# Kernel optimization log

Hardware: AMD Instinct MI355X
Metric: run time of the kernel (lower is better)

Reference implementation:

```python
import jax, jax.numpy as jnp
import numpy as np

N = 50000
E = 800000
D = 64


def sage_conv(x, src, dst, Wl, Wr, b, n_nodes):
    # message = x[src]; mean-aggregate by dst; then lin_l(mean) + lin_r(x) + b
    msg = x[src]                                             # [E, D] gather
    ssum = jax.ops.segment_sum(msg, dst, num_segments=n_nodes)  # [N, D]
    cnt = jax.ops.segment_sum(jnp.ones((msg.shape[0],), dtype=x.dtype), dst,
                              num_segments=n_nodes)          # [N]
    mean = ssum / jnp.maximum(cnt, 1.0)[:, None]             # scatter-mean (empty rows -> 0)
    return mean @ Wl.T + x @ Wr.T + b


def setup_inputs() -> dict:
    key = jax.random.key(0)
    ks = jax.random.split(key, 8)
    scale = 1.0 / np.sqrt(D)
    x = jax.random.normal(ks[0], (N, D), dtype=jnp.float32)
    edge_index = jax.random.randint(ks[1], (2, E), 0, N, dtype=jnp.int64)
    Wl1 = jax.random.normal(ks[2], (D, D), dtype=jnp.float32) * scale
    Wr1 = jax.random.normal(ks[3], (D, D), dtype=jnp.float32) * scale
    b1 = jnp.zeros((D,), dtype=jnp.float32)
    Wl2 = jax.random.normal(ks[4], (D, D), dtype=jnp.float32) * scale
    Wr2 = jax.random.normal(ks[5], (D, D), dtype=jnp.float32) * scale
    b2 = jnp.zeros((D,), dtype=jnp.float32)
    return {"x": x, "edge_index": edge_index, "Wl1": Wl1, "Wr1": Wr1, "b1": b1,
            "Wl2": Wl2, "Wr2": Wr2, "b2": b2}


def reference(x, edge_index, Wl1, Wr1, b1, Wl2, Wr2, b2):
    src, dst = edge_index[0], edge_index[1]
    n = x.shape[0]
    h = sage_conv(x, src, dst, Wl1, Wr1, b1, n)
    h = jax.nn.relu(h)
    out = sage_conv(h, src, dst, Wl2, Wr2, b2, n)
    return out
```

## Files before the change

kernel.cpp:

```cpp
#include <hip/hip_runtime.h>

#define D 64
#define CAP 64
#define WPAD 136
#define NPART 8

__device__ __forceinline__ unsigned int f2bf(float f) {
    unsigned int u = __float_as_uint(f);
    return (u + 0x7fffu + ((u >> 16) & 1u)) >> 16;
}
__device__ __forceinline__ float bflo(unsigned int u) { return __uint_as_float(u << 16); }
__device__ __forceinline__ float bfhi(unsigned int u) { return __uint_as_float(u & 0xffff0000u); }

__global__ void convert_kernel(const float* __restrict__ in,
                               unsigned short* __restrict__ outh, int total4) {
    int i = blockIdx.x * blockDim.x + threadIdx.x;
    int stride = gridDim.x * blockDim.x;
    for (; i < total4; i += stride) {
        float4 v = *reinterpret_cast<const float4*>(in + (size_t)i * 4);
        uint2 p;
        p.x = f2bf(v.x) | (f2bf(v.y) << 16);
        p.y = f2bf(v.z) | (f2bf(v.w) << 16);
        *reinterpret_cast<uint2*>(outh + (size_t)i * 4) = p;
    }
}

__global__ void fill_kernel(const int* __restrict__ src, const int* __restrict__ dst,
                            int* __restrict__ cnti, int* __restrict__ eidx,
                            int E, int N) {
    int part = blockIdx.x & (NPART - 1);
    int bip  = blockIdx.x >> 3;
    int span = (N + NPART - 1) / NPART;
    int lo = part * span;
    int hi = lo + span; if (hi > N) hi = N;
    int i = bip * blockDim.x + threadIdx.x;
    int stride = (gridDim.x >> 3) * blockDim.x;
    for (; i < E; i += stride) {
        int t = dst[i];
        if (t >= lo && t < hi) {
            int pos = atomicAdd(&cnti[t], 1);
            if (pos < CAP) eidx[(size_t)t * CAP + pos] = src[i];
        }
    }
}

__device__ __forceinline__ float dot4acc(float4 a, float4 w, float c) {
    c = fmaf(a.x, w.x, c);
    c = fmaf(a.y, w.y, c);
    c = fmaf(a.z, w.z, c);
    c = fmaf(a.w, w.w, c);
    return c;
}

__global__ __launch_bounds__(256, 4) void fused_kernel(
                             const unsigned short* __restrict__ gath,
                             const int* __restrict__ eidx,
                             const int* __restrict__ cnti,
                             const float* __restrict__ Wl,
                             const float* __restrict__ Wr,
                             const float* __restrict__ bias,
                             float* __restrict__ outf,
                             unsigned short* __restrict__ outh,
                             int do_relu, int N) {
    __shared__ unsigned short ain[64][WPAD];
    __shared__ unsigned short wsh[64][WPAD];
    __shared__ float bsh[64];
    int tid = threadIdx.x;
    int nb = blockIdx.x * 64;

    for (int c = tid; c < 64 * 32; c += 256) {
        int d = c >> 5, kc = c & 31;
        float4 v;
        if (kc < 16) v = *reinterpret_cast<const float4*>(Wl + d * D + kc * 4);
        else         v = *reinterpret_cast<const float4*>(Wr + d * D + (kc - 16) * 4);
        uint2 p;
        p.x = f2bf(v.x) | (f2bf(v.y) << 16);
        p.y = f2bf(v.z) | (f2bf(v.w) << 16);
        *reinterpret_cast<uint2*>(&wsh[d][kc * 4]) = p;
    }
    if (tid < 64) bsh[tid] = bias[tid];

    int g = tid >> 4;
    int lane = tid & 15;
    for (int ni = 0; ni < 4; ++ni) {
        int ln = ni * 16 + g;
        int node = nb + ln; if (node >= N) node = N - 1;
        int deg = cnti[node];
        int lim = deg > CAP ? CAP : deg;
        int last = lim - 1;
        const int* ep = eidx + (size_t)node * CAP;
        float4 acc = make_float4(0.f, 0.f, 0.f, 0.f);
        for (int i = 0; i < lim; i += 16) {
#define IDX(J) int e##J = ep[(i + J > last) ? last : (i + J)];
            IDX(0)  IDX(1)  IDX(2)  IDX(3)  IDX(4)  IDX(5)  IDX(6)  IDX(7)
            IDX(8)  IDX(9)  IDX(10) IDX(11) IDX(12) IDX(13) IDX(14) IDX(15)
#undef IDX
#define LD(J) uint2 w##J = *reinterpret_cast<const uint2*>(gath + (size_t)e##J * D + lane * 4);
            LD(0)  LD(1)  LD(2)  LD(3)  LD(4)  LD(5)  LD(6)  LD(7)
            LD(8)  LD(9)  LD(10) LD(11) LD(12) LD(13) LD(14) LD(15)
#undef LD
#define ACC(J) { float m = (i + J <= last) ? 1.f : 0.f;                         \
                 acc.x = fmaf(bflo(w##J.x), m, acc.x);                          \
                 acc.y = fmaf(bfhi(w##J.x), m, acc.y);                          \
                 acc.z = fmaf(bflo(w##J.y), m, acc.z);                          \
                 acc.w = fmaf(bfhi(w##J.y), m, acc.w); }
            ACC(0)  ACC(1)  ACC(2)  ACC(3)  ACC(4)  ACC(5)  ACC(6)  ACC(7)
            ACC(8)  ACC(9)  ACC(10) ACC(11) ACC(12) ACC(13) ACC(14) ACC(15)
#undef ACC
        }
        float r = 1.0f / fmaxf((float)deg, 1.0f);
        acc.x *= r; acc.y *= r; acc.z *= r; acc.w *= r;
        uint2 mp;
        mp.x = f2bf(acc.x) | (f2bf(acc.y) << 16);
        mp.y = f2bf(acc.z) | (f2bf(acc.w) << 16);
        *reinterpret_cast<uint2*>(&ain[ln][lane * 4]) = mp;
        uint2 sv = *reinterpret_cast<const uint2*>(gath + (size_t)node * D + lane * 4);
        *reinterpret_cast<uint2*>(&ain[ln][64 + lane * 4]) = sv;
    }
    __syncthreads();

    int tx = tid & 15;
    int ty = tid >> 4;

    float4 acc0 = make_float4(0.f, 0.f, 0.f, 0.f);
    float4 acc1 = make_float4(0.f, 0.f, 0.f, 0.f);
    float4 acc2 = make_float4(0.f, 0.f, 0.f, 0.f);
    float4 acc3 = make_float4(0.f, 0.f, 0.f, 0.f);

#pragma unroll 2
    for (int kc = 0; kc < 32; ++kc) {
        uint2 qa0 = *reinterpret_cast<const uint2*>(&ain[ty +  0][kc * 4]);
        uint2 qa1 = *reinterpret_cast<const uint2*>(&ain[ty + 16][kc * 4]);
        uint2 qa2 = *reinterpret_cast<const uint2*>(&ain[ty + 32][kc * 4]);
        uint2 qa3 = *reinterpret_cast<const uint2*>(&ain[ty + 48][kc * 4]);
        uint2 qw0 = *reinterpret_cast<const uint2*>(&wsh[tx +  0][kc * 4]);
        uint2 qw1 = *reinterpret_cast<const uint2*>(&wsh[tx + 16][kc * 4]);
        uint2 qw2 = *reinterpret_cast<const uint2*>(&wsh[tx + 32][kc * 4]);
        uint2 qw3 = *reinterpret_cast<const uint2*>(&wsh[tx + 48][kc * 4]);
        float4 a0 = make_float4(bflo(qa0.x), bfhi(qa0.x), bflo(qa0.y), bfhi(qa0.y));
        float4 a1 = make_float4(bflo(qa1.x), bfhi(qa1.x), bflo(qa1.y), bfhi(qa1.y));
        float4 a2 = make_float4(bflo(qa2.x), bfhi(qa2.x), bflo(qa2.y), bfhi(qa2.y));
        float4 a3 = make_float4(bflo(qa3.x), bfhi(qa3.x), bflo(qa3.y), bfhi(qa3.y));
        float4 w0 = make_float4(bflo(qw0.x), bfhi(qw0.x), bflo(qw0.y), bfhi(qw0.y));
        float4 w1 = make_float4(bflo(qw1.x), bfhi(qw1.x), bflo(qw1.y), bfhi(qw1.y));
        float4 w2 = make_float4(bflo(qw2.x), bfhi(qw2.x), bflo(qw2.y), bfhi(qw2.y));
        float4 w3 = make_float4(bflo(qw3.x), bfhi(qw3.x), bflo(qw3.y), bfhi(qw3.y));
        acc0.x = dot4acc(a0, w0, acc0.x); acc0.y = dot4acc(a0, w1, acc0.y);
        acc0.z = dot4acc(a0, w2, acc0.z); acc0.w = dot4acc(a0, w3, acc0.w);
        acc1.x = dot4acc(a1, w0, acc1.x); acc1.y = dot4acc(a1, w1, acc1.y);
        acc1.z = dot4acc(a1, w2, acc1.z); acc1.w = dot4acc(a1, w3, acc1.w);
        acc2.x = dot4acc(a2, w0, acc2.x); acc2.y = dot4acc(a2, w1, acc2.y);
        acc2.z = dot4acc(a2, w2, acc2.z); acc2.w = dot4acc(a2, w3, acc2.w);
        acc3.x = dot4acc(a3, w0, acc3.x); acc3.y = dot4acc(a3, w1, acc3.y);
        acc3.z = dot4acc(a3, w2, acc3.z); acc3.w = dot4acc(a3, w3, acc3.w);
    }

    float b0 = bsh[tx], b1 = bsh[tx + 16], b2 = bsh[tx + 32], b3 = bsh[tx + 48];
#define STORE_ROW(ACCV, I)                                                    \
    {                                                                         \
        int node = nb + ty + 16 * (I);                                        \
        if (node < N) {                                                       \
            float v0 = ACCV.x + b0, v1 = ACCV.y + b1,                         \
                  v2 = ACCV.z + b2, v3 = ACCV.w + b3;                         \
            if (do_relu) {                                                    \
                v0 = fmaxf(v0, 0.f); v1 = fmaxf(v1, 0.f);                     \
                v2 = fmaxf(v2, 0.f); v3 = fmaxf(v3, 0.f);                     \
            }                                                                 \
            if (outf) {                                                       \
                float* op = outf + (size_t)node * D;                          \
                op[tx] = v0; op[tx + 16] = v1;                                \
                op[tx + 32] = v2; op[tx + 48] = v3;                           \
            }                                                                 \
            if (outh) {                                                       \
                unsigned short* oh = outh + (size_t)node * D;                 \
                oh[tx]      = (unsigned short)f2bf(v0);                       \
                oh[tx + 16] = (unsigned short)f2bf(v1);                       \
                oh[tx + 32] = (unsigned short)f2bf(v2);                       \
                oh[tx + 48] = (unsigned short)f2bf(v3);                       \
            }                                                                 \
        }                                                                     \
    }
    STORE_ROW(acc0, 0)
    STORE_ROW(acc1, 1)
    STORE_ROW(acc2, 2)
    STORE_ROW(acc3, 3)
#undef STORE_ROW
}

extern "C" void kernel_launch(void* const* d_in, const int* in_sizes, int n_in,
                              void* d_out, int out_size, void* d_ws, size_t ws_size,
                              hipStream_t stream) {
    const float* x   = (const float*)d_in[0];
    const int*   ei  = (const int*)d_in[1];
    const float* Wl1 = (const float*)d_in[2];
    const float* Wr1 = (const float*)d_in[3];
    const float* b1  = (const float*)d_in[4];
    const float* Wl2 = (const float*)d_in[5];
    const float* Wr2 = (const float*)d_in[6];
    const float* b2  = (const float*)d_in[7];

    int N_ = in_sizes[0] / D;
    int E_ = in_sizes[1] / 2;
    const int* src = ei;
    const int* dst = ei + E_;

    int*            cnti = (int*)d_ws;
    int*            eidx = cnti + N_;
    unsigned short* xh   = (unsigned short*)(eidx + (size_t)N_ * CAP);
    unsigned short* hh   = xh + (size_t)N_ * D;
    float* outp = (float*)d_out;

    hipMemsetAsync(cnti, 0, (size_t)N_ * sizeof(int), stream);
    convert_kernel<<<2048, 256, 0, stream>>>(x, xh, N_ * D / 4);
    fill_kernel<<<2048, 256, 0, stream>>>(src, dst, cnti, eidx, E_, N_);

    int blocks = (N_ + 63) / 64;
    fused_kernel<<<blocks, 256, 0, stream>>>(xh, eidx, cnti, Wl1, Wr1, b1,
                                             (float*)nullptr, hh, 1, N_);
    fused_kernel<<<blocks, 256, 0, stream>>>(hh, eidx, cnti, Wl2, Wr2, b2,
                                             outp, (unsigned short*)nullptr, 0, N_);
}
```

Measured before the change: 212.1 us.

## Precompute bf16 weights once and halve node tile with wider gathers

Weight conversion to bf16 moves out of every fused block into a small one-off prep kernel, so each block only copies packed bf16 weights into shared memory. The node tile drops from 64 to 32 nodes per block, which doubles the block count and gives each thread one node's aggregation. Each of 8 lanes per node now gathers 16-byte rows instead of 8-byte ones, and edge indices are read as int4 vectors. This trades more blocks and more repeated weight loads per node for fewer redundant conversions and wider memory transactions in the gather.

```diff
diff --git a/kernel.cpp b/kernel.cpp
--- a/kernel.cpp
+++ b/kernel.cpp
@@ -23,6 +23,26 @@
         p.y = f2bf(v.z) | (f2bf(v.w) << 16);
         *reinterpret_cast<uint2*>(outh + (size_t)i * 4) = p;
     }
+}
+
+__global__ void wprep_kernel(const float* __restrict__ Wl1, const float* __restrict__ Wr1,
+                             const float* __restrict__ Wl2, const float* __restrict__ Wr2,
+                             unsigned short* __restrict__ wcat1,
+                             unsigned short* __restrict__ wcat2) {
+    int c = blockIdx.x * blockDim.x + threadIdx.x;
+    if (c >= 2 * 64 * 32) return;
+    int l = c >> 11, r = c & 2047;
+    int d = r >> 5, kc = r & 31;
+    const float* Wl = l ? Wl2 : Wl1;
+    const float* Wr = l ? Wr2 : Wr1;
+    float4 v;
+    if (kc < 16) v = *reinterpret_cast<const float4*>(Wl + d * D + kc * 4);
+    else         v = *reinterpret_cast<const float4*>(Wr + d * D + (kc - 16) * 4);
+    uint2 p;
+    p.x = f2bf(v.x) | (f2bf(v.y) << 16);
+    p.y = f2bf(v.z) | (f2bf(v.w) << 16);
+    unsigned short* wc = l ? wcat2 : wcat1;
+    *reinterpret_cast<uint2*>(wc + d * 128 + kc * 4) = p;
 }
 
 __global__ void fill_kernel(const int* __restrict__ src, const int* __restrict__ dst,
@@ -56,66 +76,83 @@
                              const unsigned short* __restrict__ gath,
                              const int* __restrict__ eidx,
                              const int* __restrict__ cnti,
-                             const float* __restrict__ Wl,
-                             const float* __restrict__ Wr,
+                             const unsigned short* __restrict__ wcat,
                              const float* __restrict__ bias,
                              float* __restrict__ outf,
                              unsigned short* __restrict__ outh,
                              int do_relu, int N) {
-    __shared__ unsigned short ain[64][WPAD];
+    __shared__ unsigned short ain[32][WPAD];
     __shared__ unsigned short wsh[64][WPAD];
     __shared__ float bsh[64];
     int tid = threadIdx.x;
-    int nb = blockIdx.x * 64;
-
-    for (int c = tid; c < 64 * 32; c += 256) {
+    int nb = blockIdx.x * 32;
+
+#pragma unroll
+    for (int k = 0; k < 8; ++k) {
+        int c = tid + k * 256;
         int d = c >> 5, kc = c & 31;
-        float4 v;
-        if (kc < 16) v = *reinterpret_cast<const float4*>(Wl + d * D + kc * 4);
-        else         v = *reinterpret_cast<const float4*>(Wr + d * D + (kc - 16) * 4);
-        uint2 p;
-        p.x = f2bf(v.x) | (f2bf(v.y) << 16);
-        p.y = f2bf(v.z) | (f2bf(v.w) << 16);
+        uint2 p = *reinterpret_cast<const uint2*>(wcat + d * 128 + kc * 4);
         *reinterpret_cast<uint2*>(&wsh[d][kc * 4]) = p;
     }
     if (tid < 64) bsh[tid] = bias[tid];
 
-    int g = tid >> 4;
-    int lane = tid & 15;
-    for (int ni = 0; ni < 4; ++ni) {
-        int ln = ni * 16 + g;
+    {
+        int ln = tid >> 3;
+        int lane8 = tid & 7;
         int node = nb + ln; if (node >= N) node = N - 1;
         int deg = cnti[node];
         int lim = deg > CAP ? CAP : deg;
         int last = lim - 1;
         const int* ep = eidx + (size_t)node * CAP;
-        float4 acc = make_float4(0.f, 0.f, 0.f, 0.f);
+        float ax0 = 0.f, ax1 = 0.f, ax2 = 0.f, ax3 = 0.f;
+        float ax4 = 0.f, ax5 = 0.f, ax6 = 0.f, ax7 = 0.f;
         for (int i = 0; i < lim; i += 16) {
-#define IDX(J) int e##J = ep[(i + J > last) ? last : (i + J)];
-            IDX(0)  IDX(1)  IDX(2)  IDX(3)  IDX(4)  IDX(5)  IDX(6)  IDX(7)
-            IDX(8)  IDX(9)  IDX(10) IDX(11) IDX(12) IDX(13) IDX(14) IDX(15)
-#undef IDX
-#define LD(J) uint2 w##J = *reinterpret_cast<const uint2*>(gath + (size_t)e##J * D + lane * 4);
+            int4 q0 = *reinterpret_cast<const int4*>(ep + i);
+            int4 q1 = *reinterpret_cast<const int4*>(ep + i + 4);
+            int4 q2 = *reinterpret_cast<const int4*>(ep + i + 8);
+            int4 q3 = *reinterpret_cast<const int4*>(ep + i + 12);
+            int e0 = q0.x;
+            int e1  = (i + 1  <= last) ? q0.y : e0;
+            int e2  = (i + 2  <= last) ? q0.z : e0;
+            int e3  = (i + 3  <= last) ? q0.w : e0;
+            int e4  = (i + 4  <= last) ? q1.x : e0;
+            int e5  = (i + 5  <= last) ? q1.y : e0;
+            int e6  = (i + 6  <= last) ? q1.z : e0;
+            int e7  = (i + 7  <= last) ? q1.w : e0;
+            int e8  = (i + 8  <= last) ? q2.x : e0;
+            int e9  = (i + 9  <= last) ? q2.y : e0;
+            int e10 = (i + 10 <= last) ? q2.z : e0;
+            int e11 = (i + 11 <= last) ? q2.w : e0;
+            int e12 = (i + 12 <= last) ? q3.x : e0;
+            int e13 = (i + 13 <= last) ? q3.y : e0;
+            int e14 = (i + 14 <= last) ? q3.z : e0;
+            int e15 = (i + 15 <= last) ? q3.w : e0;
+#define LD(J) uint4 w##J = *reinterpret_cast<const uint4*>(gath + (size_t)e##J * D + lane8 * 8);
             LD(0)  LD(1)  LD(2)  LD(3)  LD(4)  LD(5)  LD(6)  LD(7)
             LD(8)  LD(9)  LD(10) LD(11) LD(12) LD(13) LD(14) LD(15)
 #undef LD
-#define ACC(J) { float m = (i + J <= last) ? 1.f : 0.f;                         \
-                 acc.x = fmaf(bflo(w##J.x), m, acc.x);                          \
-                 acc.y = fmaf(bfhi(w##J.x), m, acc.y);                          \
-                 acc.z = fmaf(bflo(w##J.y), m, acc.z);                          \
-                 acc.w = fmaf(bfhi(w##J.y), m, acc.w); }
+#define ACC(J) { float m = (i + J <= last) ? 1.f : 0.f;                        \
+                 ax0 = fmaf(bflo(w##J.x), m, ax0);                             \
+                 ax1 = fmaf(bfhi(w##J.x), m, ax1);                             \
+                 ax2 = fmaf(bflo(w##J.y), m, ax2);                             \
+                 ax3 = fmaf(bfhi(w##J.y), m, ax3);                             \
+                 ax4 = fmaf(bflo(w##J.z), m, ax4);                             \
+                 ax5 = fmaf(bfhi(w##J.z), m, ax5);                             \
+                 ax6 = fmaf(bflo(w##J.w), m, ax6);                             \
+                 ax7 = fmaf(bfhi(w##J.w), m, ax7); }
             ACC(0)  ACC(1)  ACC(2)  ACC(3)  ACC(4)  ACC(5)  ACC(6)  ACC(7)
             ACC(8)  ACC(9)  ACC(10) ACC(11) ACC(12) ACC(13) ACC(14) ACC(15)
 #undef ACC
         }
         float r = 1.0f / fmaxf((float)deg, 1.0f);
-        acc.x *= r; acc.y *= r; acc.z *= r; acc.w *= r;
-        uint2 mp;
-        mp.x = f2bf(acc.x) | (f2bf(acc.y) << 16);
-        mp.y = f2bf(acc.z) | (f2bf(acc.w) << 16);
-        *reinterpret_cast<uint2*>(&ain[ln][lane * 4]) = mp;
-        uint2 sv = *reinterpret_cast<const uint2*>(gath + (size_t)node * D + lane * 4);
-        *reinterpret_cast<uint2*>(&ain[ln][64 + lane * 4]) = sv;
+        uint4 mp;
+        mp.x = f2bf(ax0 * r) | (f2bf(ax1 * r) << 16);
+        mp.y = f2bf(ax2 * r) | (f2bf(ax3 * r) << 16);
+        mp.z = f2bf(ax4 * r) | (f2bf(ax5 * r) << 16);
+        mp.w = f2bf(ax6 * r) | (f2bf(ax7 * r) << 16);
+        *reinterpret_cast<uint4*>(&ain[ln][lane8 * 8]) = mp;
+        uint4 sv = *reinterpret_cast<const uint4*>(gath + (size_t)node * D + lane8 * 8);
+        *reinterpret_cast<uint4*>(&ain[ln][64 + lane8 * 8]) = sv;
     }
     __syncthreads();
 
@@ -124,23 +161,17 @@
 
     float4 acc0 = make_float4(0.f, 0.f, 0.f, 0.f);
     float4 acc1 = make_float4(0.f, 0.f, 0.f, 0.f);
-    float4 acc2 = make_float4(0.f, 0.f, 0.f, 0.f);
-    float4 acc3 = make_float4(0.f, 0.f, 0.f, 0.f);
 
 #pragma unroll 2
     for (int kc = 0; kc < 32; ++kc) {
         uint2 qa0 = *reinterpret_cast<const uint2*>(&ain[ty +  0][kc * 4]);
         uint2 qa1 = *reinterpret_cast<const uint2*>(&ain[ty + 16][kc * 4]);
-        uint2 qa2 = *reinterpret_cast<const uint2*>(&ain[ty + 32][kc * 4]);
-        uint2 qa3 = *reinterpret_cast<const uint2*>(&ain[ty + 48][kc * 4]);
         uint2 qw0 = *reinterpret_cast<const uint2*>(&wsh[tx +  0][kc * 4]);
         uint2 qw1 = *reinterpret_cast<const uint2*>(&wsh[tx + 16][kc * 4]);
         uint2 qw2 = *reinterpret_cast<const uint2*>(&wsh[tx + 32][kc * 4]);
         uint2 qw3 = *reinterpret_cast<const uint2*>(&wsh[tx + 48][kc * 4]);
         float4 a0 = make_float4(bflo(qa0.x), bfhi(qa0.x), bflo(qa0.y), bfhi(qa0.y));
         float4 a1 = make_float4(bflo(qa1.x), bfhi(qa1.x), bflo(qa1.y), bfhi(qa1.y));
-        float4 a2 = make_float4(bflo(qa2.x), bfhi(qa2.x), bflo(qa2.y), bfhi(qa2.y));
-        float4 a3 = make_float4(bflo(qa3.x), bfhi(qa3.x), bflo(qa3.y), bfhi(qa3.y));
         float4 w0 = make_float4(bflo(qw0.x), bfhi(qw0.x), bflo(qw0.y), bfhi(qw0.y));
         float4 w1 = make_float4(bflo(qw1.x), bfhi(qw1.x), bflo(qw1.y), bfhi(qw1.y));
         float4 w2 = make_float4(bflo(qw2.x), bfhi(qw2.x), bflo(qw2.y), bfhi(qw2.y));
@@ -149,10 +180,6 @@
         acc0.z = dot4acc(a0, w2, acc0.z); acc0.w = dot4acc(a0, w3, acc0.w);
         acc1.x = dot4acc(a1, w0, acc1.x); acc1.y = dot4acc(a1, w1, acc1.y);
         acc1.z = dot4acc(a1, w2, acc1.z); acc1.w = dot4acc(a1, w3, acc1.w);
-        acc2.x = dot4acc(a2, w0, acc2.x); acc2.y = dot4acc(a2, w1, acc2.y);
-        acc2.z = dot4acc(a2, w2, acc2.z); acc2.w = dot4acc(a2, w3, acc2.w);
-        acc3.x = dot4acc(a3, w0, acc3.x); acc3.y = dot4acc(a3, w1, acc3.y);
-        acc3.z = dot4acc(a3, w2, acc3.z); acc3.w = dot4acc(a3, w3, acc3.w);
     }
 
     float b0 = bsh[tx], b1 = bsh[tx + 16], b2 = bsh[tx + 32], b3 = bsh[tx + 48];
@@ -182,8 +209,6 @@
     }
     STORE_ROW(acc0, 0)
     STORE_ROW(acc1, 1)
-    STORE_ROW(acc2, 2)
-    STORE_ROW(acc3, 3)
 #undef STORE_ROW
 }
 
@@ -204,19 +229,22 @@
     const int* src = ei;
     const int* dst = ei + E_;
 
-    int*            cnti = (int*)d_ws;
-    int*            eidx = cnti + N_;
-    unsigned short* xh   = (unsigned short*)(eidx + (size_t)N_ * CAP);
-    unsigned short* hh   = xh + (size_t)N_ * D;
+    int*            cnti  = (int*)d_ws;
+    int*            eidx  = cnti + N_;
+    unsigned short* xh    = (unsigned short*)(eidx + (size_t)N_ * CAP);
+    unsigned short* hh    = xh + (size_t)N_ * D;
+    unsigned short* wcat1 = hh + (size_t)N_ * D;
+    unsigned short* wcat2 = wcat1 + 64 * 128;
     float* outp = (float*)d_out;
 
     hipMemsetAsync(cnti, 0, (size_t)N_ * sizeof(int), stream);
     convert_kernel<<<2048, 256, 0, stream>>>(x, xh, N_ * D / 4);
+    wprep_kernel<<<16, 256, 0, stream>>>(Wl1, Wr1, Wl2, Wr2, wcat1, wcat2);
     fill_kernel<<<2048, 256, 0, stream>>>(src, dst, cnti, eidx, E_, N_);
 
-    int blocks = (N_ + 63) / 64;
-    fused_kernel<<<blocks, 256, 0, stream>>>(xh, eidx, cnti, Wl1, Wr1, b1,
+    int blocks = (N_ + 31) / 32;
+    fused_kernel<<<blocks, 256, 0, stream>>>(xh, eidx, cnti, wcat1, b1,
                                              (float*)nullptr, hh, 1, N_);
-    fused_kernel<<<blocks, 256, 0, stream>>>(hh, eidx, cnti, Wl2, Wr2, b2,
+    fused_kernel<<<blocks, 256, 0, stream>>>(hh, eidx, cnti, wcat2, b2,
                                              outp, (unsigned short*)nullptr, 0, N_);
 }
```

New measurement: 198.2 us. 1.07x faster.
